# Optimization experiments

Hardware: AMD Instinct MI355X
Metric: run time of the kernel (lower is better)

## Reference

```python
import jax, jax.numpy as jnp
import numpy as np

D_MODEL = 1024
NHEAD = 16
HEAD_DIM = D_MODEL // NHEAD  # 64
THETA = 10000.0


def apply_rope(t):
    # t: [B, H, S, D]. Interleaved-pair RoPE (lucidrains rotary-embedding-torch
    # rotate_queries_or_keys), positions = arange(S), theta = 10000.
    B, H, S, D = t.shape
    inv_freq = 1.0 / (THETA ** (jnp.arange(0, D, 2, dtype=jnp.float32) / D))  # [D/2]
    ang = jnp.arange(S, dtype=jnp.float32)[:, None] * inv_freq               # [S, D/2]
    cos = jnp.cos(ang).astype(t.dtype)
    sin = jnp.sin(ang).astype(t.dtype)
    tp = t.reshape(B, H, S, D // 2, 2)
    x1, x2 = tp[..., 0], tp[..., 1]
    rot = jnp.stack([x1 * cos - x2 * sin, x1 * sin + x2 * cos], axis=-1)
    return rot.reshape(B, H, S, D)


def setup_inputs() -> dict:
    key = jax.random.key(0)
    k0, k1, k2, k3, k4 = jax.random.split(key, 5)
    B, Sx, Sc = 2, 2048, 2048
    sc = 0.02  # weight init scale
    return {
        "x": jax.random.normal(k0, (B, Sx, D_MODEL), jnp.float32),
        "context": jax.random.normal(k1, (B, Sc, D_MODEL), jnp.float32),
        "Wq": jax.random.normal(k2, (D_MODEL, D_MODEL), jnp.float32) * sc,
        "Wv": jax.random.normal(k3, (D_MODEL, D_MODEL), jnp.float32) * sc,
        "Wo": jax.random.normal(k4, (D_MODEL, D_MODEL), jnp.float32) * sc,
        "bo": jnp.zeros((D_MODEL,), jnp.float32),
        "x_pos": jnp.arange(B * Sx, dtype=jnp.int64).reshape(B, Sx) % Sx,
        "context_pos": jnp.arange(B * Sc, dtype=jnp.int64).reshape(B, Sc) % Sc,
    }


def reference(x, context, Wq, Wv, Wo, bo, x_pos, context_pos):
    # x_pos/context_pos are unused when both streams use the internal
    # RotaryEmbedding (is_imu1=is_imu2=True), matching the original forward.
    B, Sx, _ = x.shape
    Sc = context.shape[1]
    q = (x @ Wq.T).reshape(B, Sx, NHEAD, HEAD_DIM).transpose(0, 2, 1, 3)
    # NOTE: original code uses projq (not projk) for keys — replicated here.
    k = (context @ Wq.T).reshape(B, Sc, NHEAD, HEAD_DIM).transpose(0, 2, 1, 3)
    v = (context @ Wv.T).reshape(B, Sc, NHEAD, HEAD_DIM).transpose(0, 2, 1, 3)
    q = apply_rope(q)
    k = apply_rope(k)
    scale = 1.0 / jnp.sqrt(jnp.asarray(HEAD_DIM, q.dtype))
    attn = jax.nn.softmax(jnp.einsum("bhqd,bhkd->bhqk", q, k) * scale, axis=-1)
    out = jnp.einsum("bhqk,bhkd->bhqd", attn, v)            # [B,H,Sx,hd]
    out = out.transpose(0, 2, 1, 3).reshape(B, Sx, D_MODEL)  # [B,Sx,d_model]
    return out @ Wo.T + bo
```

## Files before the change

### kernel.cpp

```cpp
#include <hip/hip_runtime.h>
#include <cmath>


typedef __bf16 bf16x8 __attribute__((ext_vector_type(8)));
typedef __bf16 bf16x4 __attribute__((ext_vector_type(4)));
typedef float f32x4 __attribute__((ext_vector_type(4)));
typedef float f32x16 __attribute__((ext_vector_type(16)));
typedef unsigned u32x4v __attribute__((ext_vector_type(4)));

#define MFMA(A, B, C) __builtin_amdgcn_mfma_f32_16x16x32_bf16(A, B, C, 0, 0, 0)
#define MFMA32(A, B, C) __builtin_amdgcn_mfma_f32_32x32x16_bf16(A, B, C, 0, 0, 0)
#define GLL16(g, l)                                                        \
  __builtin_amdgcn_global_load_lds(                                        \
      (const __attribute__((address_space(1))) unsigned int*)(g),          \
      (__attribute__((address_space(3))) unsigned int*)(l), 16, 0, 0)

#define WAITB(N)                                          \
  do {                                                    \
    asm volatile("s_waitcnt vmcnt(" #N ")" ::: "memory"); \
    __builtin_amdgcn_s_barrier();                         \
  } while (0)

__global__ __launch_bounds__(256) void cvt_all_kernel(
    const float* __restrict__ x, const float* __restrict__ ctx,
    const float* __restrict__ Wq, const float* __restrict__ Wv,
    const float* __restrict__ Wo, __bf16* __restrict__ xb, __bf16* __restrict__ cb,
    __bf16* __restrict__ Wqb, __bf16* __restrict__ Wvb, __bf16* __restrict__ Wob) {
  int base = blockIdx.x * 512 + threadIdx.x;
  const float* src;
  __bf16* dst;
  int off;
  if (base < 1048576) { src = x; dst = xb; off = 0; }
  else if (base < 2097152) { src = ctx; dst = cb; off = 1048576; }
  else if (base < 2359296) { src = Wq; dst = Wqb; off = 2097152; }
  else if (base < 2621440) { src = Wv; dst = Wvb; off = 2359296; }
  else { src = Wo; dst = Wob; off = 2621440; }
#pragma unroll
  for (int jj = 0; jj < 2; jj++) {
    int j = base - off + jj * 256;
    float4 f = ((const float4*)src)[j];
    bf16x4 o;
    o[0] = (__bf16)f.x; o[1] = (__bf16)f.y; o[2] = (__bf16)f.z; o[3] = (__bf16)f.w;
    ((bf16x4*)dst)[j] = o;
  }
}

__global__ __launch_bounds__(512, 2) void gemm_proj(const __bf16* __restrict__ A0,
                                                    const __bf16* __restrict__ W0,
                                                    void* __restrict__ outQ,
                                                    void* __restrict__ outK,
                                                    void* __restrict__ outV) {
  const int tid = threadIdx.x;
  const int wave = tid >> 6, lane = tid & 63, quad = lane >> 4, l15 = lane & 15;
  const int wm = wave >> 2, wn = wave & 3;

  const int id = blockIdx.x;
  int m0, n0;
  const __bf16* A;
  const __bf16* W;
  bool vmode;
  if (id < 128) {
    const int xcd = id & 7, j = id >> 3;
    m0 = (xcd * 4 + (j & 3)) * 256;
    n0 = (j >> 2) * 256;
    A = A0;
    W = W0;
    vmode = false;
  } else {
    const int vid = id - 128;
    const int xcd = vid & 7, j = vid >> 3;
    m0 = (xcd * 2 + (j & 1)) * 256;
    n0 = (j >> 1) * 256;
    A = A0 + (size_t)4096 * 1024;
    W = W0 + (size_t)1024 * 1024;
    vmode = true;
  }

  __shared__ __attribute__((aligned(16))) __bf16 As[4][8192];
  __shared__ __attribute__((aligned(16))) __bf16 Ws[4][8192];

  const int srow = tid >> 2;
  const int kcg = (tid & 3) ^ ((srow >> 1) & 3);
  const int aoff = srow * 1024 + kcg * 8;
  const __bf16* Ag = A + (size_t)m0 * 1024;
  const __bf16* Wg = W + (size_t)n0 * 1024;
  const int ldst = wave * 512;

  const int sw = (l15 >> 1) & 3;
  const int xoff = (quad ^ sw) * 8;

  f32x4 acc[8][4] = {};

  auto stage = [&](int t) {
    const int slot = t & 3;
    const int ko = t * 32;
    GLL16(Ag + aoff + ko,          &As[slot][ldst]);
    GLL16(Ag + aoff + 131072 + ko, &As[slot][4096 + ldst]);
    GLL16(Wg + aoff + ko,          &Ws[slot][ldst]);
    GLL16(Wg + aoff + 131072 + ko, &Ws[slot][4096 + ldst]);
  };

  auto compute = [&](int slot) {
    bf16x8 bf[4], af[4];
#pragma unroll
    for (int nf = 0; nf < 4; nf++)
      bf[nf] = *(const bf16x8*)&Ws[slot][(wn * 64 + nf * 16 + l15) * 32 + xoff];
#pragma unroll
    for (int mf = 0; mf < 4; mf++)
      af[mf] = *(const bf16x8*)&As[slot][(wm * 128 + mf * 16 + l15) * 32 + xoff];
    __builtin_amdgcn_s_setprio(1);
#pragma unroll
    for (int mf = 0; mf < 4; mf++)
#pragma unroll
      for (int nf = 0; nf < 4; nf++)
        acc[mf][nf] = MFMA(af[mf], bf[nf], acc[mf][nf]);
    __builtin_amdgcn_s_setprio(0);
#pragma unroll
    for (int mf = 0; mf < 4; mf++)
      af[mf] = *(const bf16x8*)&As[slot][(wm * 128 + (4 + mf) * 16 + l15) * 32 + xoff];
    __builtin_amdgcn_s_setprio(1);
#pragma unroll
    for (int mf = 0; mf < 4; mf++)
#pragma unroll
      for (int nf = 0; nf < 4; nf++)
        acc[4 + mf][nf] = MFMA(af[mf], bf[nf], acc[4 + mf][nf]);
    __builtin_amdgcn_s_setprio(0);
  };

  stage(0);
  stage(1);
  stage(2);
  for (int t = 0; t < 30; t++) {
    WAITB(8);
    if (t < 29) stage(t + 3);
    compute(t & 3);
  }
  WAITB(4);
  compute(2);
  WAITB(0);
  compute(3);

  if (!vmode) {
    const int isK = (m0 >= 4096);
    __bf16* O = (__bf16*)(isK ? outK : outQ);
    const float qsc = isK ? 1.0f : 0.18033688f;
    const int mb = m0 & 4095;
#pragma unroll
    for (int nf = 0; nf < 4; nf++) {
      const int n = n0 + wn * 64 + nf * 16 + l15;
      const int h = n >> 6, d = n & 63, p = d >> 1;
      const float invf_rev =
          __builtin_amdgcn_exp2f(-((float)p * 0.41524101f + 2.6514961f));
#pragma unroll
      for (int mf = 0; mf < 8; mf++) {
#pragma unroll
        for (int r = 0; r < 4; r++) {
          const int row = mb + wm * 128 + mf * 16 + quad * 4 + r;
          const int s = row & 2047, b = row >> 11;
          float v = acc[mf][nf][r];
          float pv = __shfl_xor(v, 1, 64);
          float fr = __builtin_amdgcn_fractf((float)s * invf_rev);
          float sn = __builtin_amdgcn_sinf(fr);
          float cs = __builtin_amdgcn_cosf(fr);
          float res = (lane & 1) ? (pv * sn + v * cs) : (v * cs - pv * sn);
          O[((size_t)(b * 16 + h) * 2048 + s) * 64 + d] = (__bf16)(res * qsc);
        }
      }
    }
  } else {
    __bf16* O = (__bf16*)outV;
#pragma unroll
    for (int nf = 0; nf < 4; nf++) {
      const int n = n0 + wn * 64 + nf * 16 + l15;
      const int h = n >> 6, d = n & 63;
#pragma unroll
      for (int mf = 0; mf < 8; mf++) {
        const int rowb = m0 + wm * 128 + mf * 16 + quad * 4;
        const int s = rowb & 2047, b = rowb >> 11;
        bf16x4 o;
#pragma unroll
        for (int r = 0; r < 4; r++) o[r] = (__bf16)acc[mf][nf][r];
        *(bf16x4*)(O + ((size_t)(b * 16 + h) * 64 + d) * 2048 + s) = o;
      }
    }
  }
}

__global__ __launch_bounds__(256) void gemm_out(const __bf16* __restrict__ A,
                                                const __bf16* __restrict__ W,
                                                float* __restrict__ O,
                                                const float* __restrict__ bias) {
  const int tid = threadIdx.x;
  const int wave = tid >> 6, lane = tid & 63, quad = lane >> 4, l15 = lane & 15;
  const int mw = wave >> 1, nw = wave & 1;
  const int id = blockIdx.x;
  const int xcd = id & 7, j = id >> 3;
  const int m0 = (xcd * 4 + (j & 3)) * 128;
  const int n0 = (j >> 2) * 64;

  __shared__ __attribute__((aligned(16))) __bf16 As[3][4096];
  __shared__ __attribute__((aligned(16))) __bf16 Ws[3][2048];

  int goff[2];
#pragma unroll
  for (int jj = 0; jj < 2; jj++) {
    const int s = jj * 256 + tid;
    const int row = s >> 2;
    const int kcg = (s & 3) ^ ((row >> 1) & 3);
    goff[jj] = row * 1024 + kcg * 8;
  }
  const int wrow = tid >> 2;
  const int wkcg = (tid & 3) ^ ((wrow >> 1) & 3);
  const int goffw = wrow * 1024 + wkcg * 8;

  const __bf16* Ag = A + (size_t)m0 * 1024;
  const __bf16* Wg = W + (size_t)n0 * 1024;
  const int ldsoff0 = wave * 512;
  const int ldsoff1 = 2048 + wave * 512;

  const int sw = (l15 >> 1) & 3;
  int afoff[4], wfoff[2];
#pragma unroll
  for (int t = 0; t < 4; t++)
    afoff[t] = (mw * 64 + t * 16 + l15) * 32 + (quad ^ sw) * 8;
#pragma unroll
  for (int t = 0; t < 2; t++)
    wfoff[t] = (nw * 32 + t * 16 + l15) * 32 + (quad ^ sw) * 8;

  f32x4 acc[4][2] = {};

  auto stage = [&](int buf, int k0) {
    GLL16(Ag + goff[0] + k0, &As[buf][ldsoff0]);
    GLL16(Ag + goff[1] + k0, &As[buf][ldsoff1]);
    GLL16(Wg + goffw + k0, &Ws[buf][ldsoff0]);
  };
  auto compute = [&](int buf) {
    bf16x8 af[4], wf[2];
#pragma unroll
    for (int t = 0; t < 4; t++) af[t] = *(const bf16x8*)&As[buf][afoff[t]];
#pragma unroll
    for (int t = 0; t < 2; t++) wf[t] = *(const bf16x8*)&Ws[buf][wfoff[t]];
#pragma unroll
    for (int mt = 0; mt < 4; mt++)
#pragma unroll
      for (int nt = 0; nt < 2; nt++) acc[mt][nt] = MFMA(af[mt], wf[nt], acc[mt][nt]);
  };

  stage(0, 0);
  stage(1, 32);
  int buf = 0;
  for (int c = 0; c < 32; c++) {
    __syncthreads();
    if (c + 2 < 32) {
      int nb = buf + 2;
      if (nb >= 3) nb -= 3;
      stage(nb, (c + 2) * 32);
    }
    compute(buf);
    buf = (buf == 2) ? 0 : buf + 1;
  }

#pragma unroll
  for (int nt = 0; nt < 2; nt++) {
    const int n = n0 + nw * 32 + nt * 16 + l15;
    const float bv = bias[n];
#pragma unroll
    for (int mt = 0; mt < 4; mt++) {
#pragma unroll
      for (int r = 0; r < 4; r++) {
        const int row = m0 + mw * 64 + mt * 16 + quad * 4 + r;
        O[(size_t)row * 1024 + n] = acc[mt][nt][r] + bv;
      }
    }
  }
}

__global__ __launch_bounds__(512, 4) void attn_kernel(const __bf16* __restrict__ Q,
                                                      const __bf16* __restrict__ K,
                                                      const __bf16* __restrict__ Vt,
                                                      __bf16* __restrict__ Aout) {
  const int tid = threadIdx.x;
  const int wave = tid >> 6, lane = tid & 63;
  const int l31 = lane & 31, hi = lane >> 5;
  const int qg = wave >> 1, kg = wave & 1;
  const int id = blockIdx.x;
  const int j = id >> 3;
  const int bh = ((id & 7) << 2) | (j & 3);
  const int q0 = (j >> 2) << 7;

  const __bf16* Qb = Q + (size_t)bh * (2048 * 64);
  const __bf16* Kb = K + (size_t)bh * (2048 * 64);
  const __bf16* Vb = Vt + (size_t)bh * (64 * 2048);

  __shared__ __attribute__((aligned(16))) __bf16 Kbuf[4][4096];
  __shared__ __attribute__((aligned(16))) __bf16 Vbuf[4][4096];

  bf16x8 qf[4];
  {
    const __bf16* qp = Qb + (size_t)(q0 + qg * 32 + l31) * 64 + hi * 8;
#pragma unroll
    for (int i = 0; i < 4; i++) qf[i] = *(const bf16x8*)(qp + i * 16);
  }

  const int s0 = wave * 64 + lane;
  const int r0 = s0 >> 3, c0 = (s0 & 7) ^ (r0 & 7);
  const __bf16* kgp = Kb + r0 * 64 + c0 * 8;
  const __bf16* vgp = Vb + r0 * 2048 + c0 * 8;
  const int klds = wave * 512;

  int koff[4];
  {
    const int rk = kg * 32 + l31;
#pragma unroll
    for (int i = 0; i < 4; i++) koff[i] = rk * 64 + (((2 * i + hi) ^ (rk & 7)) * 8);
  }
  int voff[2][2];
#pragma unroll
  for (int dt = 0; dt < 2; dt++) {
    const int rv = dt * 32 + l31;
#pragma unroll
    for (int ks = 0; ks < 2; ks++)
      voff[dt][ks] = rv * 64 + (((kg * 4 + ks * 2 + hi) ^ (rv & 7)) * 8);
  }

  f32x4 rs4 = {};
  f32x16 oacc[2] = {};

  auto stage = [&](int buf, int kt) {
    GLL16(kgp + kt * 64, &Kbuf[buf][klds]);
    GLL16(vgp + kt, &Vbuf[buf][klds]);
  };

  auto compute = [&](int buf) {
    f32x16 s = {};
#pragma unroll
    for (int i = 0; i < 4; i++) {
      bf16x8 kf = *(const bf16x8*)&Kbuf[buf][koff[i]];
      s = MFMA32(kf, qf[i], s);
    }
    float pe[16];
#pragma unroll
    for (int r = 0; r < 16; r++) pe[r] = __builtin_amdgcn_exp2f(s[r]);
#pragma unroll
    for (int r = 0; r < 16; r++) rs4[r & 3] += pe[r];
    bf16x8 pa[2];
#pragma unroll
    for (int sl = 0; sl < 2; sl++) {
      unsigned wa, wb, wc, wd;
      asm("v_cvt_pk_bf16_f32 %0, %1, %2" : "=v"(wa) : "v"(pe[8 * sl + 0]), "v"(pe[8 * sl + 1]));
      asm("v_cvt_pk_bf16_f32 %0, %1, %2" : "=v"(wb) : "v"(pe[8 * sl + 4]), "v"(pe[8 * sl + 5]));
      asm("v_cvt_pk_bf16_f32 %0, %1, %2" : "=v"(wc) : "v"(pe[8 * sl + 2]), "v"(pe[8 * sl + 3]));
      asm("v_cvt_pk_bf16_f32 %0, %1, %2" : "=v"(wd) : "v"(pe[8 * sl + 6]), "v"(pe[8 * sl + 7]));
      asm("v_permlane32_swap_b32 %0, %1" : "+v"(wa), "+v"(wb));
      asm("v_permlane32_swap_b32 %0, %1" : "+v"(wc), "+v"(wd));
      u32x4v t;
      t[0] = wa; t[1] = wc; t[2] = wb; t[3] = wd;
      pa[sl] = __builtin_bit_cast(bf16x8, t);
    }
#pragma unroll
    for (int dt = 0; dt < 2; dt++)
#pragma unroll
      for (int ks = 0; ks < 2; ks++) {
        bf16x8 vf = *(const bf16x8*)&Vbuf[buf][voff[dt][ks]];
        oacc[dt] = MFMA32(pa[ks], vf, oacc[dt]);
      }
  };

  stage(0, 0);
  stage(1, 64);
  for (int kt = 0; kt < 2048; kt += 128) {
    const int p = (kt >> 7) & 1;
    __syncthreads();
    if (kt + 128 < 2048) {
      stage(2 * (p ^ 1), kt + 128);
      stage(2 * (p ^ 1) + 1, kt + 192);
    }
    compute(2 * p);
    compute(2 * p + 1);
  }

  __syncthreads();
  float* Ored = (float*)&Kbuf[0][0];
  float* Lred = (float*)&Vbuf[0][0];

  float lw = (rs4[0] + rs4[1]) + (rs4[2] + rs4[3]);
  lw += __shfl_xor(lw, 32, 64);
  Lred[wave * 64 + lane] = lw;
  if (kg == 1) {
#pragma unroll
    for (int dt = 0; dt < 2; dt++)
#pragma unroll
      for (int r = 0; r < 16; r++)
        Ored[(qg * 32 + dt * 16 + r) * 64 + lane] = oacc[dt][r];
  }
  __syncthreads();
  if (kg == 0) {
    const int b = bh >> 4, h = bh & 15;
#pragma unroll
    for (int r = 0; r < 16; r++) {
      const int qrow = (r & 3) + 8 * (r >> 2) + 4 * hi;
      const float lt =
          Lred[(qg * 2) * 64 + qrow] + Lred[(qg * 2 + 1) * 64 + qrow];
      const float inv = 1.f / lt;
      const int qAbs = q0 + qg * 32 + qrow;
#pragma unroll
      for (int dt = 0; dt < 2; dt++) {
        const float o = oacc[dt][r] + Ored[(qg * 32 + dt * 16 + r) * 64 + lane];
        Aout[((size_t)(b * 2048 + qAbs)) * 1024 + h * 64 + dt * 32 + l31] =
            (__bf16)(o * inv);
      }
    }
  }
}

extern "C" void kernel_launch(void* const* d_in, const int* in_sizes, int n_in,
                              void* d_out, int out_size, void* d_ws, size_t ws_size,
                              hipStream_t stream) {
  const float* x   = (const float*)d_in[0];
  const float* ctx = (const float*)d_in[1];
  const float* Wq  = (const float*)d_in[2];
  const float* Wv  = (const float*)d_in[3];
  const float* Wo  = (const float*)d_in[4];
  const float* bo  = (const float*)d_in[5];

  char* ws = (char*)d_ws;
  const size_t MB = 1024 * 1024;
  __bf16* xb   = (__bf16*)(ws + 0 * MB);
  __bf16* cb   = (__bf16*)(ws + 8 * MB);
  __bf16* Wqb  = (__bf16*)(ws + 16 * MB);
  __bf16* Wvb  = (__bf16*)(ws + 18 * MB);
  __bf16* Wob  = (__bf16*)(ws + 20 * MB);
  __bf16* qh   = (__bf16*)(ws + 22 * MB);
  __bf16* kh   = (__bf16*)(ws + 30 * MB);
  __bf16* vt   = (__bf16*)(ws + 38 * MB);
  __bf16* attn = xb;

  cvt_all_kernel<<<5632, 256, 0, stream>>>(x, ctx, Wq, Wv, Wo, xb, cb, Wqb, Wvb, Wob);

  gemm_proj<<<192, 512, 0, stream>>>(xb, Wqb, (void*)qh, (void*)kh, (void*)vt);

  attn_kernel<<<512, 512, 0, stream>>>(qh, kh, vt, attn);

  gemm_out<<<512, 256, 0, stream>>>(attn, Wob, (float*)d_out, bo);
}
```

Before: 203.1 us.

## Restructure projection GEMM main loop into ping-pong half-tile pipeline with explicit barriers

New measurement: 201.6 us. No clear change (-0.8%).

```diff
diff --git a/kernel.cpp b/kernel.cpp
--- a/kernel.cpp
+++ b/kernel.cpp
@@ -15,11 +15,9 @@
       (const __attribute__((address_space(1))) unsigned int*)(g),          \
       (__attribute__((address_space(3))) unsigned int*)(l), 16, 0, 0)
 
-#define WAITB(N)                                          \
-  do {                                                    \
-    asm volatile("s_waitcnt vmcnt(" #N ")" ::: "memory"); \
-    __builtin_amdgcn_s_barrier();                         \
-  } while (0)
+#define VMCNT(N) asm volatile("s_waitcnt vmcnt(" #N ")" ::: "memory")
+#define BARM() asm volatile("s_barrier" ::: "memory")
+#define LGKM0() asm volatile("s_waitcnt lgkmcnt(0)" ::: "memory")
 
 __global__ __launch_bounds__(256) void cvt_all_kernel(
     const float* __restrict__ x, const float* __restrict__ ctx,
@@ -76,69 +74,99 @@
     vmode = true;
   }
 
-  __shared__ __attribute__((aligned(16))) __bf16 As[4][8192];
-  __shared__ __attribute__((aligned(16))) __bf16 Ws[4][8192];
+  __shared__ __attribute__((aligned(16))) __bf16 As[2][2][8192];
+  __shared__ __attribute__((aligned(16))) __bf16 Bs[2][2][8192];
 
   const int srow = tid >> 2;
-  const int kcg = (tid & 3) ^ ((srow >> 1) & 3);
-  const int aoff = srow * 1024 + kcg * 8;
+  const int kcg = (tid & 3) ^ (srow & 3);
+  const size_t aoff0 = (size_t)srow * 1024 + kcg * 8;
+  const size_t aoff1 = (size_t)(srow + 128) * 1024 + kcg * 8;
   const __bf16* Ag = A + (size_t)m0 * 1024;
   const __bf16* Wg = W + (size_t)n0 * 1024;
-  const int ldst = wave * 512;
-
-  const int sw = (l15 >> 1) & 3;
-  const int xoff = (quad ^ sw) * 8;
+  const int ldst0 = wave * 512;
+  const int ldst1 = 4096 + wave * 512;
+
+  auto stageA = [&](int slot, int kh, int kel) {
+    GLL16(Ag + aoff0 + kel, &As[slot][kh][ldst0]);
+    GLL16(Ag + aoff1 + kel, &As[slot][kh][ldst1]);
+  };
+  auto stageB = [&](int slot, int kh, int kel) {
+    GLL16(Wg + aoff0 + kel, &Bs[slot][kh][ldst0]);
+    GLL16(Wg + aoff1 + kel, &Bs[slot][kh][ldst1]);
+  };
+
+  const int xk = (quad ^ (l15 & 3)) * 8;
+  int afo[8], bfo[4];
+#pragma unroll
+  for (int mf = 0; mf < 8; mf++) afo[mf] = (wm * 128 + mf * 16 + l15) * 32 + xk;
+#pragma unroll
+  for (int nf = 0; nf < 4; nf++) bfo[nf] = (wn * 64 + nf * 16 + l15) * 32 + xk;
 
   f32x4 acc[8][4] = {};
-
-  auto stage = [&](int t) {
-    const int slot = t & 3;
-    const int ko = t * 32;
-    GLL16(Ag + aoff + ko,          &As[slot][ldst]);
-    GLL16(Ag + aoff + 131072 + ko, &As[slot][4096 + ldst]);
-    GLL16(Wg + aoff + ko,          &Ws[slot][ldst]);
-    GLL16(Wg + aoff + 131072 + ko, &Ws[slot][4096 + ldst]);
-  };
-
-  auto compute = [&](int slot) {
-    bf16x8 bf[4], af[4];
-#pragma unroll
-    for (int nf = 0; nf < 4; nf++)
-      bf[nf] = *(const bf16x8*)&Ws[slot][(wn * 64 + nf * 16 + l15) * 32 + xoff];
+  bf16x8 bf[4], af[4];
+
+  auto loadB = [&](int slot, int kh) {
+#pragma unroll
+    for (int nf = 0; nf < 4; nf++) bf[nf] = *(const bf16x8*)&Bs[slot][kh][bfo[nf]];
+  };
+  auto loadA = [&](int slot, int kh, int mfg) {
 #pragma unroll
     for (int mf = 0; mf < 4; mf++)
-      af[mf] = *(const bf16x8*)&As[slot][(wm * 128 + mf * 16 + l15) * 32 + xoff];
+      af[mf] = *(const bf16x8*)&As[slot][kh][afo[mfg * 4 + mf]];
+  };
+  auto mfma16 = [&](int mfg) {
     __builtin_amdgcn_s_setprio(1);
 #pragma unroll
     for (int mf = 0; mf < 4; mf++)
 #pragma unroll
       for (int nf = 0; nf < 4; nf++)
-        acc[mf][nf] = MFMA(af[mf], bf[nf], acc[mf][nf]);
+        acc[mfg * 4 + mf][nf] = MFMA(af[mf], bf[nf], acc[mfg * 4 + mf][nf]);
     __builtin_amdgcn_s_setprio(0);
-#pragma unroll
-    for (int mf = 0; mf < 4; mf++)
-      af[mf] = *(const bf16x8*)&As[slot][(wm * 128 + (4 + mf) * 16 + l15) * 32 + xoff];
-    __builtin_amdgcn_s_setprio(1);
-#pragma unroll
-    for (int mf = 0; mf < 4; mf++)
-#pragma unroll
-      for (int nf = 0; nf < 4; nf++)
-        acc[4 + mf][nf] = MFMA(af[mf], bf[nf], acc[4 + mf][nf]);
-    __builtin_amdgcn_s_setprio(0);
-  };
-
-  stage(0);
-  stage(1);
-  stage(2);
-  for (int t = 0; t < 30; t++) {
-    WAITB(8);
-    if (t < 29) stage(t + 3);
-    compute(t & 3);
-  }
-  WAITB(4);
-  compute(2);
-  WAITB(0);
-  compute(3);
+  };
+
+  stageA(0, 0, 0);  stageB(0, 0, 0);
+  stageA(0, 1, 32); stageB(0, 1, 32);
+  stageA(1, 0, 64); stageB(1, 0, 64);
+  VMCNT(8); BARM();
+
+#pragma unroll 1
+  for (int j = 0; j < 7; j++) {
+    const int kb = j * 128;
+    loadB(0, 0); loadA(0, 0, 0); stageA(1, 1, kb + 96);
+    BARM(); LGKM0(); mfma16(0); BARM();
+    loadA(0, 0, 1); stageB(1, 1, kb + 96);
+    BARM(); LGKM0(); mfma16(1); VMCNT(8); BARM();
+    loadB(0, 1); loadA(0, 1, 0); stageA(0, 0, kb + 128);
+    BARM(); LGKM0(); mfma16(0); BARM();
+    loadA(0, 1, 1); stageB(0, 0, kb + 128);
+    BARM(); LGKM0(); mfma16(1); VMCNT(8); BARM();
+    loadB(1, 0); loadA(1, 0, 0); stageA(0, 1, kb + 160);
+    BARM(); LGKM0(); mfma16(0); BARM();
+    loadA(1, 0, 1); stageB(0, 1, kb + 160);
+    BARM(); LGKM0(); mfma16(1); VMCNT(8); BARM();
+    loadB(1, 1); loadA(1, 1, 0); stageA(1, 0, kb + 192);
+    BARM(); LGKM0(); mfma16(0); BARM();
+    loadA(1, 1, 1); stageB(1, 0, kb + 192);
+    BARM(); LGKM0(); mfma16(1); VMCNT(8); BARM();
+  }
+  {
+    loadB(0, 0); loadA(0, 0, 0); stageA(1, 1, 992);
+    BARM(); LGKM0(); mfma16(0); BARM();
+    loadA(0, 0, 1); stageB(1, 1, 992);
+    BARM(); LGKM0(); mfma16(1); VMCNT(8); BARM();
+    loadB(0, 1); loadA(0, 1, 0);
+    BARM(); LGKM0(); mfma16(0); BARM();
+    loadA(0, 1, 1);
+    BARM(); LGKM0(); mfma16(1); VMCNT(4); BARM();
+    loadB(1, 0); loadA(1, 0, 0);
+    BARM(); LGKM0(); mfma16(0); BARM();
+    loadA(1, 0, 1);
+    BARM(); LGKM0(); mfma16(1); VMCNT(0); BARM();
+    loadB(1, 1); loadA(1, 1, 0);
+    BARM(); LGKM0(); mfma16(0); BARM();
+    loadA(1, 1, 1);
+    BARM(); LGKM0(); mfma16(1);
+  }
 
   if (!vmode) {
     const int isK = (m0 >= 4096);
```
